# Optimization experiments

Measured on AMD Instinct MI355X. Metric: run time of the kernel, lower is better.

The kernel has to match this reference:

```python
import jax, jax.numpy as jnp
import numpy as np

B, S, E = 4, 2048, 1024
H = E // 2  # per-head dim (2 heads)


def setup_inputs() -> dict:
    key = jax.random.key(0)
    ks = jax.random.split(key, 10)
    w = 0.02
    return {
        "input": jax.random.normal(ks[0], (B, S, E), dtype=jnp.float32),
        "Wq": jax.random.normal(ks[1], (2, H, H), dtype=jnp.float32) * w,
        "bq": jax.random.normal(ks[2], (2, H), dtype=jnp.float32) * w,
        "Wk": jax.random.normal(ks[3], (2, H, H), dtype=jnp.float32) * w,
        "bk": jax.random.normal(ks[4], (2, H), dtype=jnp.float32) * w,
        "Wv": jax.random.normal(ks[5], (2, H, H), dtype=jnp.float32) * w,
        "bv": jax.random.normal(ks[6], (2, H), dtype=jnp.float32) * w,
        "Wf": jax.random.normal(ks[7], (E, E), dtype=jnp.float32) * w,
        "bf": jax.random.normal(ks[8], (E,), dtype=jnp.float32) * w,
        "masked": 1,
    }


def reference(input, Wq, bq, Wk, bk, Wv, bv, Wf, bf, masked):
    b, s, e = input.shape
    h = e // 2
    # contiguous split into 2 heads: [b, s, 2, h]
    xh = input.reshape(b, s, 2, h)
    # per-head Linear: y = x @ W.T + b  (W is [out, in])
    q = jnp.einsum("bsnh,noh->bsno", xh, Wq) + bq
    k = jnp.einsum("bsnh,noh->bsno", xh, Wk) + bk
    v = jnp.einsum("bsnh,noh->bsno", xh, Wv) + bv
    # scores: [b, n, s, t]
    scores = jnp.einsum("bsno,btno->bnst", q, k) / jnp.sqrt(jnp.float32(h))
    if masked:
        causal = jnp.tril(jnp.ones((s, s), dtype=bool))
        scores = jnp.where(causal, scores, jnp.float32(-jnp.inf))
    probs = jax.nn.softmax(scores, axis=-1)
    out = jnp.einsum("bnst,btnh->bsnh", probs, v).reshape(b, s, e)
    return jnp.einsum("bse,oe->bso", out, Wf) + bf
```

## Files before the change

kernel.cpp:

```cpp
#include <hip/hip_runtime.h>
#include <hip/hip_bf16.h>

#define BB 4
#define SS 2048
#define EE 1024
#define HH 512

typedef __attribute__((ext_vector_type(8))) short short8;
typedef __attribute__((ext_vector_type(4))) float f32x4;

static __device__ __forceinline__ unsigned short f2bf(float x){
  unsigned u = __float_as_uint(x);
  u += 0x7fffu + ((u >> 16) & 1u);
  return (unsigned short)(u >> 16);
}

static __device__ __forceinline__ void gload16(const void* g, void* l){
  __builtin_amdgcn_global_load_lds((const __attribute__((address_space(1))) void*)g,
                                   (__attribute__((address_space(3))) void*)l, 16, 0, 0);
}

__global__ void k_cvt(const float* __restrict__ in, unsigned short* __restrict__ out, int n8){
  int idx = blockIdx.x * blockDim.x + threadIdx.x;
  int stride = gridDim.x * blockDim.x;
  for (int i = idx; i < n8; i += stride){
    const float4* p = (const float4*)in + (long)i * 2;
    float4 a = p[0], b = p[1];
    union { unsigned short u[8]; uint4 v; } r;
    r.u[0]=f2bf(a.x); r.u[1]=f2bf(a.y); r.u[2]=f2bf(a.z); r.u[3]=f2bf(a.w);
    r.u[4]=f2bf(b.x); r.u[5]=f2bf(b.y); r.u[6]=f2bf(b.z); r.u[7]=f2bf(b.w);
    ((uint4*)out)[i] = r.v;
  }
}

#define GBK 32

template<bool OUT_BF16>
static __device__ __forceinline__ void gemm_tile(
    const unsigned short* __restrict__ A, int lda,
    const unsigned short* __restrict__ Bw, int ldb,
    void* __restrict__ Cc, int ldc,
    const float* __restrict__ bias, int K, int row0, int col0, float oscale)
{
  __shared__ unsigned short As[2][128 * GBK];
  __shared__ unsigned short Bs[2][128 * GBK];
  const int tid = threadIdx.x, lane = tid & 63, w = tid >> 6;
  const int wm = w >> 1, wn = w & 1;
  const int fr = lane & 15, g = lane >> 4;

  f32x4 acc[4][4];
  #pragma unroll
  for (int i = 0; i < 4; i++)
    #pragma unroll
    for (int j = 0; j < 4; j++){ acc[i][j][0]=0.f; acc[i][j][1]=0.f; acc[i][j][2]=0.f; acc[i][j][3]=0.f; }

  const unsigned short* gAsrc[2]; const unsigned short* gBsrc[2];
  unsigned ldsOff[2];
  #pragma unroll
  for (int i = 0; i < 2; i++){
    int slot = w*128 + i*64 + lane;
    int row = slot >> 2, ch = slot & 3;
    int sc_ = ch ^ ((row >> 1) & 3);
    gAsrc[i] = A  + (long)(row0 + row) * lda + sc_ * 8;
    gBsrc[i] = Bw + (long)(col0 + row) * ldb + sc_ * 8;
    ldsOff[i] = (unsigned)((w*128 + i*64) * 8);
  }

  unsigned aoff[4], boff[4];
  #pragma unroll
  for (int mi = 0; mi < 4; mi++){
    int row = wm*64 + mi*16 + fr;
    aoff[mi] = row * GBK + ((g ^ ((row >> 1) & 3)) * 8);
  }
  #pragma unroll
  for (int ni = 0; ni < 4; ni++){
    int row = wn*64 + ni*16 + fr;
    boff[ni] = row * GBK + ((g ^ ((row >> 1) & 3)) * 8);
  }

  const int KT = K / GBK;
  #pragma unroll
  for (int i = 0; i < 2; i++) gload16(gAsrc[i], &As[0][ldsOff[i]]);
  #pragma unroll
  for (int i = 0; i < 2; i++) gload16(gBsrc[i], &Bs[0][ldsOff[i]]);
  __syncthreads();

  for (int kt = 0; kt < KT; ++kt){
    const int cur = kt & 1;
    if (kt + 1 < KT){
      #pragma unroll
      for (int i = 0; i < 2; i++) gload16(gAsrc[i] + (kt+1)*GBK, &As[cur^1][ldsOff[i]]);
      #pragma unroll
      for (int i = 0; i < 2; i++) gload16(gBsrc[i] + (kt+1)*GBK, &Bs[cur^1][ldsOff[i]]);
    }
    short8 av[4], bv[4];
    #pragma unroll
    for (int mi = 0; mi < 4; mi++) av[mi] = *(const short8*)&As[cur][aoff[mi]];
    #pragma unroll
    for (int ni = 0; ni < 4; ni++) bv[ni] = *(const short8*)&Bs[cur][boff[ni]];
    #pragma unroll
    for (int mi = 0; mi < 4; mi++)
      #pragma unroll
      for (int ni = 0; ni < 4; ni++)
        acc[mi][ni] = __builtin_amdgcn_mfma_f32_16x16x32_bf16(av[mi], bv[ni], acc[mi][ni], 0, 0, 0);
    __syncthreads();
  }

  #pragma unroll
  for (int mi = 0; mi < 4; mi++){
    #pragma unroll
    for (int ni = 0; ni < 4; ni++){
      int row = row0 + wm*64 + mi*16 + g*4;
      int col = col0 + wn*64 + ni*16 + fr;
      float bb = bias[col];
      #pragma unroll
      for (int r = 0; r < 4; r++){
        float v = (acc[mi][ni][r] + bb) * oscale;
        if (OUT_BF16) ((unsigned short*)Cc)[(long)(row + r) * ldc + col] = f2bf(v);
        else          ((float*)Cc)[(long)(row + r) * ldc + col] = v;
      }
    }
  }
}

__global__ __launch_bounds__(256, 2) void k_qkv(
    const unsigned short* __restrict__ xb,
    const unsigned short* __restrict__ wq, const unsigned short* __restrict__ wk,
    const unsigned short* __restrict__ wv,
    const float* __restrict__ bq, const float* __restrict__ bk, const float* __restrict__ bv,
    unsigned short* __restrict__ Q, unsigned short* __restrict__ K, unsigned short* __restrict__ V)
{
  int z = blockIdx.z; int which = z >> 3; int bn = z & 7; int b = bn >> 1, n = bn & 1;
  const unsigned short* W; const float* bias; unsigned short* out;
  float os = 1.f;
  if (which == 0){ W = wq; bias = bq; out = Q; os = 0.044194173824159216f; }
  else if (which == 1){ W = wk; bias = bk; out = K; }
  else { W = wv; bias = bv; out = V; }
  W += n * HH * HH; bias += n * HH; out += (long)bn * SS * HH;
  const unsigned short* Ap = xb + (long)b * SS * EE + n * HH;
  gemm_tile<true>(Ap, EE, W, HH, out, HH, bias, HH, blockIdx.x * 128, blockIdx.y * 128, os);
}

__global__ __launch_bounds__(256, 2) void k_outproj(
    const unsigned short* __restrict__ O, const unsigned short* __restrict__ wf,
    const float* __restrict__ bfb, float* __restrict__ out)
{
  gemm_tile<false>(O, EE, wf, EE, out, EE, bfb, EE, blockIdx.x * 128, blockIdx.y * 128, 1.f);
}

__global__ __launch_bounds__(256) void k_transpose(const unsigned short* __restrict__ V,
                                                   unsigned short* __restrict__ Vt){
  __shared__ unsigned short t[64 * 64];
  long base = (long)blockIdx.z * SS * HH;
  const unsigned short* in = V + base;
  unsigned short* out = Vt + base;
  int s0 = blockIdx.x * 64, o0 = blockIdx.y * 64;
  int tid = threadIdx.x;
  int r = tid >> 3, cch = tid & 7;
  #pragma unroll
  for (int p = 0; p < 2; p++){
    int s = p * 32 + r;
    uint4 v = *(const uint4*)&in[(long)(s0 + s) * HH + o0 + cch * 8];
    *(uint4*)&t[s * 64 + ((cch ^ ((s >> 3) & 7)) * 8)] = v;
  }
  __syncthreads();
  #pragma unroll
  for (int p = 0; p < 2; p++){
    int o = p * 32 + r;
    union { unsigned short u[8]; uint4 v; } x;
    #pragma unroll
    for (int j = 0; j < 8; j++){
      int s = cch * 8 + j;
      x.u[j] = t[s * 64 + (((o >> 3) ^ ((s >> 3) & 7)) * 8) + (o & 7)];
    }
    *(uint4*)&out[(long)(o0 + o) * SS + s0 + cch * 8] = x.v;
  }
}

#define QB 128
#define TB 32

__global__ __launch_bounds__(512, 2) void k_flash3(
    const unsigned short* __restrict__ Qg, const unsigned short* __restrict__ Kg,
    const unsigned short* __restrict__ Vtg,
    unsigned short* __restrict__ Opart, float* __restrict__ mlg,
    const int* __restrict__ maskedp)
{
  __shared__ unsigned short Ks[2][TB * HH];
  __shared__ unsigned short Vs[2][HH * TB];
  __shared__ unsigned short Ps[8][16][TB + 8];

  const int bid = blockIdx.x;
  const int bn = bid & 7;
  const int u = bid >> 3;
  const int masked = *maskedp;
  int qi, c;
  if (masked){
    qi = -1; c = 0;
    int cnt = 0;
    #pragma unroll 1
    for (int q = 0; q < 16; q++){
      int nch = (4*q + 27) / 24;
      if (qi < 0 && u >= cnt && u < cnt + nch){ qi = q; c = u - cnt; }
      cnt += nch;
    }
    if (qi < 0) return;
  } else { qi = u >> 1; c = u & 1; }
  const int n  = masked ? 4*qi + 4 : 64;
  const int CH = masked ? 24 : 32;
  const int t0 = c * CH;
  const int t1 = min(n, t0 + CH);

  const long base = (long)bn * SS * HH;
  const unsigned short* Qp = Qg + base;
  const unsigned short* Kp = Kg + base;
  const unsigned short* Vp = Vtg + base;

  const int tid = threadIdx.x, lane = tid & 63, w = tid >> 6;
  const int fr = lane & 15, g = lane >> 4;
  const int q0 = qi * QB;

  short8 Qr[16];
  {
    const unsigned short* qrow = Qp + (long)(q0 + w * 16 + fr) * HH + g * 8;
    #pragma unroll
    for (int kk = 0; kk < 16; kk++) Qr[kk] = *(const short8*)(qrow + kk * 32);
  }

  f32x4 Oacc[32];
  #pragma unroll
  for (int i = 0; i < 32; i++){ Oacc[i][0]=0.f; Oacc[i][1]=0.f; Oacc[i][2]=0.f; Oacc[i][3]=0.f; }
  float m_r[4], l_r[4];
  #pragma unroll
  for (int r = 0; r < 4; r++){ m_r[r] = -1e30f; l_r[r] = 0.f; }

  auto stage = [&](int buf, int t){
    #pragma unroll
    for (int i = 0; i < 8; i++){
      const int sbase = w * 512 + i * 64;
      const int slot = sbase + lane;
      if (sbase < 2048){
        int row = slot >> 6, ch = slot & 63;
        int sc_ = ch ^ (row & 7);
        gload16(Kp + (long)(t * TB + row) * HH + sc_ * 8, &Ks[buf][sbase * 8]);
      } else {
        int s2 = slot - 2048;
        int row = s2 >> 2, ch = s2 & 3;
        int sc_ = ch ^ ((row >> 1) & 3);
        gload16(Vp + (long)row * SS + t * TB + sc_ * 8, &Vs[buf][(s2 - lane) * 8 + lane * 8]);
      }
    }
  };

  stage(0, t0);
  __syncthreads();

  for (int t = t0; t < t1; ++t){
    const int cur = (t - t0) & 1;
    if (t + 1 < t1) stage(cur ^ 1, t + 1);

    f32x4 sc[2];
    #pragma unroll
    for (int tf = 0; tf < 2; tf++){ sc[tf][0]=0.f; sc[tf][1]=0.f; sc[tf][2]=0.f; sc[tf][3]=0.f; }
    #pragma unroll
    for (int kk = 0; kk < 16; kk++){
      #pragma unroll
      for (int tf = 0; tf < 2; tf++){
        int row = tf * 16 + fr;
        short8 kf = *(const short8*)&Ks[cur][row * HH + (((kk * 4 + g) ^ (row & 7)) * 8)];
        sc[tf] = __builtin_amdgcn_mfma_f32_16x16x32_bf16(Qr[kk], kf, sc[tf], 0, 0, 0);
      }
    }

    const bool needmask = masked && (t * TB + TB - 1 > q0 + w * 16);
    if (needmask){
      #pragma unroll
      for (int tf = 0; tf < 2; tf++){
        int col = t * TB + tf * 16 + fr;
        #pragma unroll
        for (int r = 0; r < 4; r++){
          int row = q0 + w * 16 + g * 4 + r;
          if (col > row) sc[tf][r] = -1e30f;
        }
      }
    }

    float mx[4];
    #pragma unroll
    for (int r = 0; r < 4; r++) mx[r] = fmaxf(sc[0][r], sc[1][r]);
    #pragma unroll
    for (int d = 1; d < 16; d <<= 1){
      #pragma unroll
      for (int r = 0; r < 4; r++) mx[r] = fmaxf(mx[r], __shfl_xor(mx[r], d, 64));
    }
    bool grow = false;
    #pragma unroll
    for (int r = 0; r < 4; r++) grow = grow || (mx[r] > m_r[r] + 8.f);
    if (__any(grow)){
      float alpha[4];
      #pragma unroll
      for (int r = 0; r < 4; r++){
        float mn = fmaxf(m_r[r], mx[r]);
        alpha[r] = __expf(m_r[r] - mn);
        m_r[r] = mn;
        l_r[r] *= alpha[r];
      }
      #pragma unroll
      for (int i = 0; i < 32; i++)
        #pragma unroll
        for (int r = 0; r < 4; r++) Oacc[i][r] *= alpha[r];
    }

    float ps[4] = {0.f, 0.f, 0.f, 0.f};
    #pragma unroll
    for (int tf = 0; tf < 2; tf++)
      #pragma unroll
      for (int r = 0; r < 4; r++){
        float p = __expf(sc[tf][r] - m_r[r]);
        sc[tf][r] = p;
        ps[r] += p;
      }
    #pragma unroll
    for (int d = 1; d < 16; d <<= 1){
      #pragma unroll
      for (int r = 0; r < 4; r++) ps[r] += __shfl_xor(ps[r], d, 64);
    }
    #pragma unroll
    for (int r = 0; r < 4; r++) l_r[r] += ps[r];

    #pragma unroll
    for (int tf = 0; tf < 2; tf++)
      #pragma unroll
      for (int r = 0; r < 4; r++)
        Ps[w][g * 4 + r][tf * 16 + fr] = f2bf(sc[tf][r]);

    short8 pa = *(const short8*)&Ps[w][fr][g * 8];
    #pragma unroll
    for (int hf = 0; hf < 32; ++hf){
      int row = hf * 16 + fr;
      short8 vf = *(const short8*)&Vs[cur][row * TB + ((g ^ ((row >> 1) & 3)) * 8)];
      Oacc[hf] = __builtin_amdgcn_mfma_f32_16x16x32_bf16(pa, vf, Oacc[hf], 0, 0, 0);
    }
    __syncthreads();
  }

  const long slot = (long)(bn * 16 + qi) * 3 + c;
  unsigned short* dst = Opart + slot * (QB * HH);
  #pragma unroll
  for (int hf = 0; hf < 32; ++hf){
    int col = hf * 16 + fr;
    #pragma unroll
    for (int r = 0; r < 4; r++)
      dst[(w * 16 + g * 4 + r) * HH + col] = f2bf(Oacc[hf][r]);
  }
  if (fr == 0){
    #pragma unroll
    for (int r = 0; r < 4; r++){
      int row = w * 16 + g * 4 + r;
      mlg[slot * 256 + row]       = m_r[r];
      mlg[slot * 256 + 128 + row] = l_r[r];
    }
  }
}

__global__ __launch_bounds__(256) void k_combine(
    const unsigned short* __restrict__ Opart, const float* __restrict__ mlg,
    unsigned short* __restrict__ O, const int* __restrict__ maskedp)
{
  __shared__ float wl[128][3];
  const int gq = blockIdx.x;
  const int bn = gq & 7, qi = gq >> 3;
  const int b = bn >> 1, n = bn & 1;
  const int NC = (*maskedp) ? (4*qi + 27) / 24 : 2;
  const long slotbase = (long)(bn * 16 + qi) * 3;
  const int tid = threadIdx.x;

  if (tid < 128){
    float mc[3], lc[3];
    float M = -1e30f;
    for (int c = 0; c < NC; c++){
      mc[c] = mlg[(slotbase + c) * 256 + tid];
      lc[c] = mlg[(slotbase + c) * 256 + 128 + tid];
      M = fmaxf(M, mc[c]);
    }
    float L = 0.f;
    for (int c = 0; c < NC; c++){
      float wc = __expf(mc[c] - M);
      mc[c] = wc;
      L += lc[c] * wc;
    }
    float inv = 1.f / L;
    #pragma unroll
    for (int c = 0; c < 3; c++) wl[tid][c] = (c < NC) ? mc[c] * inv : 0.f;
  }
  __syncthreads();

  for (int it = 0; it < 32; it++){
    int idx = it * 256 + tid;
    int row = idx >> 6, cv = idx & 63;
    float acc[8] = {0.f,0.f,0.f,0.f,0.f,0.f,0.f,0.f};
    for (int c = 0; c < NC; c++){
      float wc = wl[row][c];
      short8 v = *(const short8*)&Opart[(slotbase + c) * (QB * HH) + row * HH + cv * 8];
      #pragma unroll
      for (int j = 0; j < 8; j++){
        float f = __uint_as_float((unsigned)(unsigned short)v[j] << 16);
        acc[j] += f * wc;
      }
    }
    union { unsigned short u[8]; uint4 q; } rr;
    #pragma unroll
    for (int j = 0; j < 8; j++) rr.u[j] = f2bf(acc[j]);
    long dstoff = ((long)b * SS + qi * QB + row) * EE + n * HH + cv * 8;
    *(uint4*)&O[dstoff] = rr.q;
  }
}

extern "C" void kernel_launch(void* const* d_in, const int* in_sizes, int n_in,
                              void* d_out, int out_size, void* d_ws, size_t ws_size,
                              hipStream_t stream)
{
  const float* x   = (const float*)d_in[0];
  const float* Wq  = (const float*)d_in[1];
  const float* bq  = (const float*)d_in[2];
  const float* Wk  = (const float*)d_in[3];
  const float* bk  = (const float*)d_in[4];
  const float* Wv  = (const float*)d_in[5];
  const float* bv  = (const float*)d_in[6];
  const float* Wf  = (const float*)d_in[7];
  const float* bf_ = (const float*)d_in[8];
  const int* masked = (const int*)d_in[9];

  char* p = (char*)d_ws;
  const long TEN = (long)BB * SS * EE * 2;
  unsigned short* xb  = (unsigned short*)p; p += TEN;
  unsigned short* Qb  = (unsigned short*)p; p += TEN;
  unsigned short* Kb  = (unsigned short*)p; p += TEN;
  unsigned short* Vb  = (unsigned short*)p; p += TEN;
  unsigned short* wqb = (unsigned short*)p; p += 2L * HH * HH * 2;
  unsigned short* wkb = (unsigned short*)p; p += 2L * HH * HH * 2;
  unsigned short* wvb = (unsigned short*)p; p += 2L * HH * HH * 2;
  unsigned short* wfb = (unsigned short*)p; p += (long)EE * EE * 2;
  unsigned short* Opart = (unsigned short*)p; p += 384L * QB * HH * 2;
  float* mlg = (float*)p; p += 384L * 256 * 4;

  k_cvt<<<dim3(2048), 256, 0, stream>>>(x,  xb,  BB * SS * EE / 8);
  k_cvt<<<dim3(256),  256, 0, stream>>>(Wq, wqb, 2 * HH * HH / 8);
  k_cvt<<<dim3(256),  256, 0, stream>>>(Wk, wkb, 2 * HH * HH / 8);
  k_cvt<<<dim3(256),  256, 0, stream>>>(Wv, wvb, 2 * HH * HH / 8);
  k_cvt<<<dim3(512),  256, 0, stream>>>(Wf, wfb, EE * EE / 8);

  k_qkv<<<dim3(SS / 128, HH / 128, 24), 256, 0, stream>>>(xb, wqb, wkb, wvb, bq, bk, bv, Qb, Kb, Vb);
  k_transpose<<<dim3(SS / 64, HH / 64, 8), 256, 0, stream>>>(Vb, xb);
  k_flash3<<<dim3(256), 512, 0, stream>>>(Qb, Kb, xb, Opart, mlg, masked);
  k_combine<<<dim3(128), 256, 0, stream>>>(Opart, mlg, Vb, masked);
  k_outproj<<<dim3((BB * SS) / 128, EE / 128, 1), 256, 0, stream>>>(Vb, wfb, bf_, (float*)d_out);
}
```

Measured before the change: 270.9 us.

## Split PV accumulation by head-dim columns per wave and share probabilities via LDS

The PV stage is repartitioned. Each wave now owns a 64-column slice of the head dimension for all 128 query rows, instead of all 512 columns for its own 16 rows. Each wave loads its V fragments into registers once and reuses them across the 8 row groups, reading every wave's probabilities and per-row rescale factors from shared memory. An extra barrier is needed before PV, so the next tile's prefetch now starts after the score phase, which shortens the overlap window. The alpha rescale of the accumulators now runs every iteration instead of only when the row max grows.

```diff
diff --git a/kernel.cpp b/kernel.cpp
--- a/kernel.cpp
+++ b/kernel.cpp
@@ -180,7 +180,7 @@
 #define QB 128
 #define TB 32
 
-__global__ __launch_bounds__(512, 2) void k_flash3(
+__global__ __launch_bounds__(512, 2) void k_flash5(
     const unsigned short* __restrict__ Qg, const unsigned short* __restrict__ Kg,
     const unsigned short* __restrict__ Vtg,
     unsigned short* __restrict__ Opart, float* __restrict__ mlg,
@@ -189,6 +189,7 @@
   __shared__ unsigned short Ks[2][TB * HH];
   __shared__ unsigned short Vs[2][HH * TB];
   __shared__ unsigned short Ps[8][16][TB + 8];
+  __shared__ float Al[8][16];
 
   const int bid = blockIdx.x;
   const int bn = bid & 7;
@@ -227,9 +228,11 @@
     for (int kk = 0; kk < 16; kk++) Qr[kk] = *(const short8*)(qrow + kk * 32);
   }
 
-  f32x4 Oacc[32];
-  #pragma unroll
-  for (int i = 0; i < 32; i++){ Oacc[i][0]=0.f; Oacc[i][1]=0.f; Oacc[i][2]=0.f; Oacc[i][3]=0.f; }
+  f32x4 Oacc[8][4];
+  #pragma unroll
+  for (int i = 0; i < 8; i++)
+    #pragma unroll
+    for (int j = 0; j < 4; j++){ Oacc[i][j][0]=0.f; Oacc[i][j][1]=0.f; Oacc[i][j][2]=0.f; Oacc[i][j][3]=0.f; }
   float m_r[4], l_r[4];
   #pragma unroll
   for (int r = 0; r < 4; r++){ m_r[r] = -1e30f; l_r[r] = 0.f; }
@@ -247,7 +250,7 @@
         int s2 = slot - 2048;
         int row = s2 >> 2, ch = s2 & 3;
         int sc_ = ch ^ ((row >> 1) & 3);
-        gload16(Vp + (long)row * SS + t * TB + sc_ * 8, &Vs[buf][(s2 - lane) * 8 + lane * 8]);
+        gload16(Vp + (long)row * SS + t * TB + sc_ * 8, &Vs[buf][(sbase - 2048) * 8]);
       }
     }
   };
@@ -257,7 +260,6 @@
 
   for (int t = t0; t < t1; ++t){
     const int cur = (t - t0) & 1;
-    if (t + 1 < t1) stage(cur ^ 1, t + 1);
 
     f32x4 sc[2];
     #pragma unroll
@@ -293,23 +295,23 @@
       #pragma unroll
       for (int r = 0; r < 4; r++) mx[r] = fmaxf(mx[r], __shfl_xor(mx[r], d, 64));
     }
+    float alpha[4];
     bool grow = false;
     #pragma unroll
     for (int r = 0; r < 4; r++) grow = grow || (mx[r] > m_r[r] + 8.f);
     if (__any(grow)){
-      float alpha[4];
       #pragma unroll
       for (int r = 0; r < 4; r++){
         float mn = fmaxf(m_r[r], mx[r]);
         alpha[r] = __expf(m_r[r] - mn);
         m_r[r] = mn;
-        l_r[r] *= alpha[r];
-      }
-      #pragma unroll
-      for (int i = 0; i < 32; i++)
-        #pragma unroll
-        for (int r = 0; r < 4; r++) Oacc[i][r] *= alpha[r];
-    }
+      }
+    } else {
+      #pragma unroll
+      for (int r = 0; r < 4; r++) alpha[r] = 1.f;
+    }
+    #pragma unroll
+    for (int r = 0; r < 4; r++) l_r[r] *= alpha[r];
 
     float ps[4] = {0.f, 0.f, 0.f, 0.f};
     #pragma unroll
@@ -333,25 +335,48 @@
       #pragma unroll
       for (int r = 0; r < 4; r++)
         Ps[w][g * 4 + r][tf * 16 + fr] = f2bf(sc[tf][r]);
-
-    short8 pa = *(const short8*)&Ps[w][fr][g * 8];
-    #pragma unroll
-    for (int hf = 0; hf < 32; ++hf){
-      int row = hf * 16 + fr;
-      short8 vf = *(const short8*)&Vs[cur][row * TB + ((g ^ ((row >> 1) & 3)) * 8)];
-      Oacc[hf] = __builtin_amdgcn_mfma_f32_16x16x32_bf16(pa, vf, Oacc[hf], 0, 0, 0);
-    }
+    if (fr == 0){
+      #pragma unroll
+      for (int r = 0; r < 4; r++) Al[w][g * 4 + r] = alpha[r];
+    }
+
+    __syncthreads();
+
+    if (t + 1 < t1) stage(cur ^ 1, t + 1);
+
+    short8 vf[4];
+    #pragma unroll
+    for (int hf = 0; hf < 4; hf++){
+      int row = w * 64 + hf * 16 + fr;
+      vf[hf] = *(const short8*)&Vs[cur][row * TB + ((g ^ ((row >> 1) & 3)) * 8)];
+    }
+    #pragma unroll
+    for (int rw = 0; rw < 8; rw++){
+      f32x4 alr = *(const f32x4*)&Al[rw][g * 4];
+      #pragma unroll
+      for (int hf = 0; hf < 4; hf++)
+        #pragma unroll
+        for (int r = 0; r < 4; r++) Oacc[rw][hf][r] *= alr[r];
+      short8 pa = *(const short8*)&Ps[rw][fr][g * 8];
+      #pragma unroll
+      for (int hf = 0; hf < 4; hf++)
+        Oacc[rw][hf] = __builtin_amdgcn_mfma_f32_16x16x32_bf16(pa, vf[hf], Oacc[rw][hf], 0, 0, 0);
+    }
+
     __syncthreads();
   }
 
   const long slot = (long)(bn * 16 + qi) * 3 + c;
   unsigned short* dst = Opart + slot * (QB * HH);
   #pragma unroll
-  for (int hf = 0; hf < 32; ++hf){
-    int col = hf * 16 + fr;
-    #pragma unroll
-    for (int r = 0; r < 4; r++)
-      dst[(w * 16 + g * 4 + r) * HH + col] = f2bf(Oacc[hf][r]);
+  for (int rw = 0; rw < 8; rw++){
+    #pragma unroll
+    for (int hf = 0; hf < 4; hf++){
+      int col = w * 64 + hf * 16 + fr;
+      #pragma unroll
+      for (int r = 0; r < 4; r++)
+        dst[(rw * 16 + g * 4 + r) * HH + col] = f2bf(Oacc[rw][hf][r]);
+    }
   }
   if (fr == 0){
     #pragma unroll
@@ -452,7 +477,7 @@
 
   k_qkv<<<dim3(SS / 128, HH / 128, 24), 256, 0, stream>>>(xb, wqb, wkb, wvb, bq, bk, bv, Qb, Kb, Vb);
   k_transpose<<<dim3(SS / 64, HH / 64, 8), 256, 0, stream>>>(Vb, xb);
-  k_flash3<<<dim3(256), 512, 0, stream>>>(Qb, Kb, xb, Opart, mlg, masked);
+  k_flash5<<<dim3(256), 512, 0, stream>>>(Qb, Kb, xb, Opart, mlg, masked);
   k_combine<<<dim3(128), 256, 0, stream>>>(Opart, mlg, Vb, masked);
   k_outproj<<<dim3((BB * SS) / 128, EE / 128, 1), 256, 0, stream>>>(Vb, wfb, bf_, (float*)d_out);
 }
```

Result: slower. 278.6 us (+2.9%).

## Restructure flash attention to 32x32 MFMA with split head-dim warps

Applied to the files above, without the earlier changes.

Rewrites the flash attention kernel to use 32x32x16 bf16 MFMAs. Each pair of warps splits the 512-wide head dimension in half, and their partial QK scores are summed through shared memory. The P operand is now built in registers with packed bf16 conversion and cross-lane shuffles instead of a shared-memory round trip. V is single-buffered and staged by the upper four warps while the lower four stage K. The causal chunk size also changes from 24 to 22, with the combine kernel updated to match. In exchange it adds an extra barrier per tile, drops the launch-bounds occupancy hint to 1, and the single V buffer risks exposing load latency.

```diff
diff --git a/kernel.cpp b/kernel.cpp
--- a/kernel.cpp
+++ b/kernel.cpp
@@ -8,11 +8,18 @@
 
 typedef __attribute__((ext_vector_type(8))) short short8;
 typedef __attribute__((ext_vector_type(4))) float f32x4;
+typedef __attribute__((ext_vector_type(16))) float f32x16;
 
 static __device__ __forceinline__ unsigned short f2bf(float x){
   unsigned u = __float_as_uint(x);
   u += 0x7fffu + ((u >> 16) & 1u);
   return (unsigned short)(u >> 16);
+}
+
+static __device__ __forceinline__ unsigned cvtpk(float lo, float hi){
+  unsigned d;
+  asm("v_cvt_pk_bf16_f32 %0, %1, %2" : "=v"(d) : "v"(lo), "v"(hi));
+  return d;
 }
 
 static __device__ __forceinline__ void gload16(const void* g, void* l){
@@ -180,15 +187,15 @@
 #define QB 128
 #define TB 32
 
-__global__ __launch_bounds__(512, 2) void k_flash3(
+__global__ __launch_bounds__(512, 1) void k_flash7(
     const unsigned short* __restrict__ Qg, const unsigned short* __restrict__ Kg,
     const unsigned short* __restrict__ Vtg,
     unsigned short* __restrict__ Opart, float* __restrict__ mlg,
     const int* __restrict__ maskedp)
 {
   __shared__ unsigned short Ks[2][TB * HH];
-  __shared__ unsigned short Vs[2][HH * TB];
-  __shared__ unsigned short Ps[8][16][TB + 8];
+  __shared__ unsigned short Vs[HH * TB];
+  __shared__ float2 Sx[4][2][8][64];
 
   const int bid = blockIdx.x;
   const int bn = bid & 7;
@@ -200,14 +207,14 @@
     int cnt = 0;
     #pragma unroll 1
     for (int q = 0; q < 16; q++){
-      int nch = (4*q + 27) / 24;
+      int nch = (4*q + 25) / 22;
       if (qi < 0 && u >= cnt && u < cnt + nch){ qi = q; c = u - cnt; }
       cnt += nch;
     }
     if (qi < 0) return;
   } else { qi = u >> 1; c = u & 1; }
   const int n  = masked ? 4*qi + 4 : 64;
-  const int CH = masked ? 24 : 32;
+  const int CH = masked ? 22 : 32;
   const int t0 = c * CH;
   const int t1 = min(n, t0 + CH);
 
@@ -217,149 +224,150 @@
   const unsigned short* Vp = Vtg + base;
 
   const int tid = threadIdx.x, lane = tid & 63, w = tid >> 6;
-  const int fr = lane & 15, g = lane >> 4;
+  const int ln = lane & 31, hi = lane >> 5;
+  const int rg = w & 3, dh = w >> 2;
   const int q0 = qi * QB;
+  const int myq = q0 + rg * 32 + ln;
 
   short8 Qr[16];
   {
-    const unsigned short* qrow = Qp + (long)(q0 + w * 16 + fr) * HH + g * 8;
-    #pragma unroll
-    for (int kk = 0; kk < 16; kk++) Qr[kk] = *(const short8*)(qrow + kk * 32);
-  }
-
-  f32x4 Oacc[32];
-  #pragma unroll
-  for (int i = 0; i < 32; i++){ Oacc[i][0]=0.f; Oacc[i][1]=0.f; Oacc[i][2]=0.f; Oacc[i][3]=0.f; }
-  float m_r[4], l_r[4];
-  #pragma unroll
-  for (int r = 0; r < 4; r++){ m_r[r] = -1e30f; l_r[r] = 0.f; }
-
-  auto stage = [&](int buf, int t){
-    #pragma unroll
-    for (int i = 0; i < 8; i++){
-      const int sbase = w * 512 + i * 64;
-      const int slot = sbase + lane;
-      if (sbase < 2048){
+    const unsigned short* qrow = Qp + (long)myq * HH + dh * 256 + hi * 8;
+    #pragma unroll
+    for (int ks = 0; ks < 16; ks++) Qr[ks] = *(const short8*)(qrow + ks * 16);
+  }
+
+  f32x16 oa[8];
+  #pragma unroll
+  for (int i = 0; i < 8; i++)
+    #pragma unroll
+    for (int r = 0; r < 16; r++) oa[i][r] = 0.f;
+  float m_r = -1e30f, l_r = 0.f;
+
+  auto stageK = [&](int buf, int t){
+    if (w < 4){
+      #pragma unroll
+      for (int i = 0; i < 8; i++){
+        const int sbase = w * 512 + i * 64;
+        const int slot = sbase + lane;
         int row = slot >> 6, ch = slot & 63;
         int sc_ = ch ^ (row & 7);
         gload16(Kp + (long)(t * TB + row) * HH + sc_ * 8, &Ks[buf][sbase * 8]);
-      } else {
-        int s2 = slot - 2048;
-        int row = s2 >> 2, ch = s2 & 3;
+      }
+    }
+  };
+  auto stageV = [&](int t){
+    if (w >= 4){
+      #pragma unroll
+      for (int i = 0; i < 8; i++){
+        const int sbase = (w - 4) * 512 + i * 64;
+        const int slot = sbase + lane;
+        int row = slot >> 2, ch = slot & 3;
         int sc_ = ch ^ ((row >> 1) & 3);
-        gload16(Vp + (long)row * SS + t * TB + sc_ * 8, &Vs[buf][(s2 - lane) * 8 + lane * 8]);
+        gload16(Vp + (long)row * SS + t * TB + sc_ * 8, &Vs[sbase * 8]);
       }
     }
   };
 
-  stage(0, t0);
+  stageK(0, t0);
+  stageV(t0);
   __syncthreads();
 
   for (int t = t0; t < t1; ++t){
     const int cur = (t - t0) & 1;
-    if (t + 1 < t1) stage(cur ^ 1, t + 1);
-
-    f32x4 sc[2];
-    #pragma unroll
-    for (int tf = 0; tf < 2; tf++){ sc[tf][0]=0.f; sc[tf][1]=0.f; sc[tf][2]=0.f; sc[tf][3]=0.f; }
-    #pragma unroll
-    for (int kk = 0; kk < 16; kk++){
-      #pragma unroll
-      for (int tf = 0; tf < 2; tf++){
-        int row = tf * 16 + fr;
-        short8 kf = *(const short8*)&Ks[cur][row * HH + (((kk * 4 + g) ^ (row & 7)) * 8)];
-        sc[tf] = __builtin_amdgcn_mfma_f32_16x16x32_bf16(Qr[kk], kf, sc[tf], 0, 0, 0);
-      }
-    }
-
-    const bool needmask = masked && (t * TB + TB - 1 > q0 + w * 16);
-    if (needmask){
-      #pragma unroll
-      for (int tf = 0; tf < 2; tf++){
-        int col = t * TB + tf * 16 + fr;
+    if (t > t0)     stageV(t);
+    if (t + 1 < t1) stageK(cur ^ 1, t + 1);
+
+    f32x16 sa;
+    #pragma unroll
+    for (int r = 0; r < 16; r++) sa[r] = 0.f;
+    #pragma unroll
+    for (int ks = 0; ks < 16; ks++){
+      int ch = (dh * 32 + ks * 2 + hi) ^ (ln & 7);
+      short8 kf = *(const short8*)&Ks[cur][ln * HH + ch * 8];
+      sa = __builtin_amdgcn_mfma_f32_32x32x16_bf16(kf, Qr[ks], sa, 0, 0, 0);
+    }
+
+    #pragma unroll
+    for (int i = 0; i < 8; i++)
+      Sx[rg][dh][i][lane] = make_float2(sa[2*i], sa[2*i+1]);
+
+    __syncthreads();
+
+    float p[16];
+    #pragma unroll
+    for (int i = 0; i < 8; i++){
+      float2 o = Sx[rg][dh ^ 1][i][lane];
+      p[2*i]   = sa[2*i]   + o.x;
+      p[2*i+1] = sa[2*i+1] + o.y;
+    }
+
+    if (masked && (t * TB + TB - 1 > myq)){
+      #pragma unroll
+      for (int r = 0; r < 16; r++){
+        int tl = (r & 3) + 8 * (r >> 2) + 4 * hi;
+        if (t * TB + tl > myq) p[r] = -1e30f;
+      }
+    }
+
+    float mx = p[0];
+    #pragma unroll
+    for (int r = 1; r < 16; r++) mx = fmaxf(mx, p[r]);
+    mx = fmaxf(mx, __shfl_xor(mx, 32, 64));
+    if (__any(mx > m_r + 8.f)){
+      float mn = fmaxf(m_r, mx);
+      float alpha = __expf(m_r - mn);
+      m_r = mn; l_r *= alpha;
+      #pragma unroll
+      for (int r = 0; r < 16; r++){
+        float al = __shfl(alpha, (r & 3) + 8 * (r >> 2) + 4 * hi, 64);
         #pragma unroll
-        for (int r = 0; r < 4; r++){
-          int row = q0 + w * 16 + g * 4 + r;
-          if (col > row) sc[tf][r] = -1e30f;
-        }
-      }
-    }
-
-    float mx[4];
-    #pragma unroll
-    for (int r = 0; r < 4; r++) mx[r] = fmaxf(sc[0][r], sc[1][r]);
-    #pragma unroll
-    for (int d = 1; d < 16; d <<= 1){
-      #pragma unroll
-      for (int r = 0; r < 4; r++) mx[r] = fmaxf(mx[r], __shfl_xor(mx[r], d, 64));
-    }
-    bool grow = false;
-    #pragma unroll
-    for (int r = 0; r < 4; r++) grow = grow || (mx[r] > m_r[r] + 8.f);
-    if (__any(grow)){
-      float alpha[4];
-      #pragma unroll
-      for (int r = 0; r < 4; r++){
-        float mn = fmaxf(m_r[r], mx[r]);
-        alpha[r] = __expf(m_r[r] - mn);
-        m_r[r] = mn;
-        l_r[r] *= alpha[r];
-      }
-      #pragma unroll
-      for (int i = 0; i < 32; i++)
-        #pragma unroll
-        for (int r = 0; r < 4; r++) Oacc[i][r] *= alpha[r];
-    }
-
-    float ps[4] = {0.f, 0.f, 0.f, 0.f};
-    #pragma unroll
-    for (int tf = 0; tf < 2; tf++)
-      #pragma unroll
-      for (int r = 0; r < 4; r++){
-        float p = __expf(sc[tf][r] - m_r[r]);
-        sc[tf][r] = p;
-        ps[r] += p;
-      }
-    #pragma unroll
-    for (int d = 1; d < 16; d <<= 1){
-      #pragma unroll
-      for (int r = 0; r < 4; r++) ps[r] += __shfl_xor(ps[r], d, 64);
-    }
-    #pragma unroll
-    for (int r = 0; r < 4; r++) l_r[r] += ps[r];
-
-    #pragma unroll
-    for (int tf = 0; tf < 2; tf++)
-      #pragma unroll
-      for (int r = 0; r < 4; r++)
-        Ps[w][g * 4 + r][tf * 16 + fr] = f2bf(sc[tf][r]);
-
-    short8 pa = *(const short8*)&Ps[w][fr][g * 8];
-    #pragma unroll
-    for (int hf = 0; hf < 32; ++hf){
-      int row = hf * 16 + fr;
-      short8 vf = *(const short8*)&Vs[cur][row * TB + ((g ^ ((row >> 1) & 3)) * 8)];
-      Oacc[hf] = __builtin_amdgcn_mfma_f32_16x16x32_bf16(pa, vf, Oacc[hf], 0, 0, 0);
-    }
+        for (int i = 0; i < 8; i++) oa[i][r] *= al;
+      }
+    }
+    float ps = 0.f;
+    #pragma unroll
+    for (int r = 0; r < 16; r++){ float pe = __expf(p[r] - m_r); p[r] = pe; ps += pe; }
+    ps += __shfl_xor(ps, 32, 64);
+    l_r += ps;
+
+    unsigned W[8], R[8];
+    #pragma unroll
+    for (int i = 0; i < 8; i++) W[i] = cvtpk(p[2*i], p[2*i+1]);
+    #pragma unroll
+    for (int i = 0; i < 8; i++) R[i] = __shfl_xor(W[i], 32, 64);
+    union { unsigned u[4]; short8 s; } fa0, fa1;
+    fa0.u[0] = hi ? R[2] : W[0];  fa0.u[1] = hi ? R[3] : W[1];
+    fa0.u[2] = hi ? W[2] : R[0];  fa0.u[3] = hi ? W[3] : R[1];
+    fa1.u[0] = hi ? R[6] : W[4];  fa1.u[1] = hi ? R[7] : W[5];
+    fa1.u[2] = hi ? W[6] : R[4];  fa1.u[3] = hi ? W[7] : R[5];
+
+    #pragma unroll
+    for (int cf = 0; cf < 8; cf++){
+      int h = dh * 256 + cf * 32 + ln;
+      int sw = (h >> 1) & 3;
+      short8 v0 = *(const short8*)&Vs[h * TB + ((hi     ^ sw) * 8)];
+      oa[cf] = __builtin_amdgcn_mfma_f32_32x32x16_bf16(fa0.s, v0, oa[cf], 0, 0, 0);
+      short8 v1 = *(const short8*)&Vs[h * TB + (((2+hi) ^ sw) * 8)];
+      oa[cf] = __builtin_amdgcn_mfma_f32_32x32x16_bf16(fa1.s, v1, oa[cf], 0, 0, 0);
+    }
+
     __syncthreads();
   }
 
   const long slot = (long)(bn * 16 + qi) * 3 + c;
   unsigned short* dst = Opart + slot * (QB * HH);
   #pragma unroll
-  for (int hf = 0; hf < 32; ++hf){
-    int col = hf * 16 + fr;
-    #pragma unroll
-    for (int r = 0; r < 4; r++)
-      dst[(w * 16 + g * 4 + r) * HH + col] = f2bf(Oacc[hf][r]);
-  }
-  if (fr == 0){
-    #pragma unroll
-    for (int r = 0; r < 4; r++){
-      int row = w * 16 + g * 4 + r;
-      mlg[slot * 256 + row]       = m_r[r];
-      mlg[slot * 256 + 128 + row] = l_r[r];
-    }
+  for (int cf = 0; cf < 8; cf++){
+    int col = dh * 256 + cf * 32 + ln;
+    #pragma unroll
+    for (int r = 0; r < 16; r++){
+      int row = rg * 32 + (r & 3) + 8 * (r >> 2) + 4 * hi;
+      dst[row * HH + col] = f2bf(oa[cf][r]);
+    }
+  }
+  if (w < 4 && hi == 0){
+    mlg[slot * 256 + rg * 32 + ln]       = m_r;
+    mlg[slot * 256 + 128 + rg * 32 + ln] = l_r;
   }
 }
 
@@ -371,7 +379,7 @@
   const int gq = blockIdx.x;
   const int bn = gq & 7, qi = gq >> 3;
   const int b = bn >> 1, n = bn & 1;
-  const int NC = (*maskedp) ? (4*qi + 27) / 24 : 2;
+  const int NC = (*maskedp) ? (4*qi + 25) / 22 : 2;
   const long slotbase = (long)(bn * 16 + qi) * 3;
   const int tid = threadIdx.x;
 
@@ -452,7 +460,7 @@
 
   k_qkv<<<dim3(SS / 128, HH / 128, 24), 256, 0, stream>>>(xb, wqb, wkb, wvb, bq, bk, bv, Qb, Kb, Vb);
   k_transpose<<<dim3(SS / 64, HH / 64, 8), 256, 0, stream>>>(Vb, xb);
-  k_flash3<<<dim3(256), 512, 0, stream>>>(Qb, Kb, xb, Opart, mlg, masked);
+  k_flash7<<<dim3(256), 512, 0, stream>>>(Qb, Kb, xb, Opart, mlg, masked);
   k_combine<<<dim3(128), 256, 0, stream>>>(Opart, mlg, Vb, masked);
   k_outproj<<<dim3((BB * SS) / 128, EE / 128, 1), 256, 0, stream>>>(Vb, wfb, bf_, (float*)d_out);
 }
```

After: 237.8 us. 1.14x faster.
